# Performance work log

Measured on AMD Instinct MI355X. Metric: run time of the kernel, lower is better.

## Reference

```python
import jax, jax.numpy as jnp
import numpy as np

D, DFF, H, B, L, S = 1024, 4096, 16, 4, 1024, 1024


def setup_inputs() -> dict:
    key = jax.random.key(0)
    ks = jax.random.split(key, 8)
    w = lambda k, shape, s=0.02: jax.random.normal(k, shape, jnp.float32) * s
    return {
        'x': jax.random.normal(ks[0], (B, L, D), jnp.float32),
        'xa': jax.random.normal(ks[1], (B, S, D), jnp.float32),
        'sa_in_w': w(ks[2], (3 * D, D)), 'sa_in_b': jnp.zeros((3 * D,), jnp.float32),
        'sa_out_w': w(ks[3], (D, D)), 'sa_out_b': jnp.zeros((D,), jnp.float32),
        'ln1_w': jnp.ones((D,), jnp.float32), 'ln1_b': jnp.zeros((D,), jnp.float32),
        'ca_in_w': w(ks[4], (3 * D, D)), 'ca_in_b': jnp.zeros((3 * D,), jnp.float32),
        'ca_out_w': w(ks[5], (D, D)), 'ca_out_b': jnp.zeros((D,), jnp.float32),
        'ln2_w': jnp.ones((D,), jnp.float32), 'ln2_b': jnp.zeros((D,), jnp.float32),
        'ff_w1': w(ks[6], (DFF, D)), 'ff_b1': jnp.zeros((DFF,), jnp.float32),
        'ff_w2': w(ks[7], (D, DFF)), 'ff_b2': jnp.zeros((D,), jnp.float32),
        'ln3_w': jnp.ones((D,), jnp.float32), 'ln3_b': jnp.zeros((D,), jnp.float32),
    }


def layer_norm(x, w, b, eps=1e-5):
    m = x.mean(-1, keepdims=True)
    v = ((x - m) ** 2).mean(-1, keepdims=True)
    return (x - m) * jax.lax.rsqrt(v + eps) * w + b


def mha(q_in, kv_in, in_w, in_b, out_w, out_b):
    # torch MultiheadAttention eager path; returns (out, head-averaged weights)
    wq, wk, wv = jnp.split(in_w, 3, axis=0)
    bq, bk, bv = jnp.split(in_b, 3, axis=0)
    Bq, Lq, Dm = q_in.shape
    Lk = kv_in.shape[1]
    dh = Dm // H
    q = (q_in @ wq.T + bq).reshape(Bq, Lq, H, dh)
    k = (kv_in @ wk.T + bk).reshape(Bq, Lk, H, dh)
    v = (kv_in @ wv.T + bv).reshape(Bq, Lk, H, dh)
    scores = jnp.einsum('blhd,bshd->bhls', q, k) / jnp.sqrt(jnp.asarray(dh, q.dtype))
    attn = jax.nn.softmax(scores, axis=-1)  # [B,H,L,S]
    out = jnp.einsum('bhls,bshd->blhd', attn, v).reshape(Bq, Lq, Dm)
    return out @ out_w.T + out_b, attn.mean(axis=1)


def reference(x, xa, sa_in_w, sa_in_b, sa_out_w, sa_out_b, ln1_w, ln1_b,
              ca_in_w, ca_in_b, ca_out_w, ca_out_b, ln2_w, ln2_b,
              ff_w1, ff_b1, ff_w2, ff_b2, ln3_w, ln3_b):
    # NOTE: module overwrites x with LN(x) before the residual add
    x = layer_norm(x, ln1_w, ln1_b)
    a, self_w = mha(x, x, sa_in_w, sa_in_b, sa_out_w, sa_out_b)
    x = x + a
    x = layer_norm(x, ln2_w, ln2_b)
    a, cross_w = mha(x, xa, ca_in_w, ca_in_b, ca_out_w, ca_out_b)
    x = x + a
    h = layer_norm(x, ln3_w, ln3_b)
    x = x + (jax.nn.gelu(h @ ff_w1.T + ff_b1, approximate=False) @ ff_w2.T + ff_b2)
    return (x, jax.lax.stop_gradient(self_w), jax.lax.stop_gradient(cross_w))
```

## Files before the change

### kernel.cpp

```cpp
#include <hip/hip_runtime.h>
#include <cstdint>
#include <cstddef>


#define DEVI __device__ __forceinline__

typedef unsigned short u16;
typedef unsigned int u32;
typedef float f32x4 __attribute__((ext_vector_type(4)));
typedef short bf16x8 __attribute__((ext_vector_type(8)));

DEVI float bf2f(u16 u) { union { u32 i; float f; } x; x.i = ((u32)u) << 16; return x.f; }
DEVI u16 f2bf(float f) {
  union { float f; u32 i; } x; x.f = f;
  u32 r = x.i + 0x7fffu + ((x.i >> 16) & 1u);
  return (u16)(r >> 16);
}
DEVI u32 cvtpk(float lo, float hi) {
  u32 r;
  asm("v_cvt_pk_bf16_f32 %0, %1, %2" : "=v"(r) : "v"(lo), "v"(hi));
  return r;
}
DEVI float unplo(u32 u) { union { u32 i; float f; } x; x.i = u << 16; return x.f; }
DEVI float unphi(u32 u) { union { u32 i; float f; } x; x.i = u & 0xffff0000u; return x.f; }

typedef const __attribute__((address_space(1))) void GV;
typedef __attribute__((address_space(3))) void LV;
DEVI void glds16(const void* g, void* l) {
  __builtin_amdgcn_global_load_lds((GV*)g, (LV*)l, 16, 0, 0);
}

struct ConvBatch {
  const float* src[7];
  u16* dst[7];
  int n[7];
};

__global__ __launch_bounds__(256) void conv_batch(ConvBatch cb) {
  int t = blockIdx.y;
  const float* __restrict__ in = cb.src[t];
  u16* __restrict__ out = cb.dst[t];
  int n = cb.n[t];
  int i = (blockIdx.x * 256 + threadIdx.x) * 4;
  int stride = gridDim.x * 256 * 4;
  for (; i < n; i += stride) {
    float4 v = *(const float4*)(in + i);
    ushort4 o; o.x = f2bf(v.x); o.y = f2bf(v.y); o.z = f2bf(v.z); o.w = f2bf(v.w);
    *(ushort4*)(out + i) = o;
  }
}

__global__ __launch_bounds__(256) void ln_kernel(const float* __restrict__ in,
                                                 const float* __restrict__ gw,
                                                 const float* __restrict__ gb,
                                                 float* __restrict__ o32,
                                                 u16* __restrict__ o16) {
  int row = blockIdx.x;
  int t = threadIdx.x;
  const float* p = in + ((size_t)row << 10);
  float4 v = *(const float4*)(p + t * 4);
  float s = v.x + v.y + v.z + v.w;
  float q = v.x * v.x + v.y * v.y + v.z * v.z + v.w * v.w;
#pragma unroll
  for (int off = 32; off; off >>= 1) { s += __shfl_xor(s, off, 64); q += __shfl_xor(q, off, 64); }
  __shared__ float sb[8];
  int lane = t & 63, wv = t >> 6;
  if (!lane) { sb[wv] = s; sb[4 + wv] = q; }
  __syncthreads();
  s = sb[0] + sb[1] + sb[2] + sb[3];
  q = sb[4] + sb[5] + sb[6] + sb[7];
  float mean = s * (1.f / 1024.f);
  float var = q * (1.f / 1024.f) - mean * mean;
  float rs = rsqrtf(var + 1e-5f);
  float4 w4 = *(const float4*)(gw + t * 4);
  float4 b4 = *(const float4*)(gb + t * 4);
  float y0 = (v.x - mean) * rs * w4.x + b4.x;
  float y1 = (v.y - mean) * rs * w4.y + b4.y;
  float y2 = (v.z - mean) * rs * w4.z + b4.z;
  float y3 = (v.w - mean) * rs * w4.w + b4.w;
  float4 o; o.x = y0; o.y = y1; o.z = y2; o.w = y3;
  *(float4*)(o32 + ((size_t)row << 10) + t * 4) = o;
  ushort4 ob; ob.x = f2bf(y0); ob.y = f2bf(y1); ob.z = f2bf(y2); ob.w = f2bf(y3);
  *(ushort4*)(o16 + ((size_t)row << 10) + t * 4) = ob;
}

__global__ __launch_bounds__(256) void transpose_v(const u16* __restrict__ src, u16* __restrict__ dst) {
  __shared__ u16 tile[64][72];
  int bh = blockIdx.y;
  int b = bh >> 4, h = bh & 15;
  int s0 = blockIdx.x * 64;
  int t = threadIdx.x;
#pragma unroll
  for (int p = 0; p < 4; ++p) {
    int s = p * 16 + (t >> 4);
    int d = (t & 15) * 4;
    ushort4 v = *(const ushort4*)(src + ((size_t)(b * 1024 + s0 + s)) * 3072 + h * 64 + d);
    tile[s][d] = v.x; tile[s][d + 1] = v.y; tile[s][d + 2] = v.z; tile[s][d + 3] = v.w;
  }
  __syncthreads();
#pragma unroll
  for (int p = 0; p < 4; ++p) {
    int d = p * 16 + (t >> 4);
    int s = (t & 15) * 4;
    ushort4 v;
    v.x = tile[s][d]; v.y = tile[s + 1][d]; v.z = tile[s + 2][d]; v.w = tile[s + 3][d];
    *(ushort4*)(dst + ((size_t)(bh * 64 + d)) * 1024 + s0 + s) = v;
  }
}

__global__ __launch_bounds__(256, 4) void attn_fused2(const u16* __restrict__ qkv,
                                                      const u16* __restrict__ vT,
                                                      u16* __restrict__ probs,
                                                      u16* __restrict__ attnv) {
  __shared__ __align__(16) char LdsRaw[17408];
  __shared__ float wredm[4][2][16];
  __shared__ float wreds[4][2][16];
  u16* Kst = (u16*)LdsRaw;
  float* Ored = (float*)LdsRaw;

  const int hbid = blockIdx.y * 32 + blockIdx.x;
  const int lbid = (hbid & 7) * 256 + (hbid >> 3);
  const int z = lbid >> 5, b = z >> 4, h = z & 15;
  const int l0 = (lbid & 31) * 32;
  const int tid = threadIdx.x, lane = tid & 63, w = tid >> 6;
  const int fr = lane & 15, c16 = lane >> 4;

  bf16x8 qf[2][2];
#pragma unroll
  for (int i = 0; i < 2; ++i)
#pragma unroll
    for (int kk = 0; kk < 2; ++kk)
      qf[i][kk] = *(const bf16x8*)(qkv + (size_t)(b * 1024 + l0 + 16 * i + fr) * 3072 +
                                   h * 64 + kk * 32 + c16 * 8);

  const u16* Kbase = qkv + (size_t)b * 1024 * 3072 + 1024 + h * 64;

  u32 pk[2][16][2];
  float mx0 = -1e30f, mx1 = -1e30f;

#pragma unroll
  for (int cc = 0; cc < 8; ++cc) {
#pragma unroll
    for (int it = 0; it < 4; ++it) {
      int n = it * 256 + tid;
      int kk = n >> 9, r = (n >> 2) & 127, un = n & 3;
      int su = un ^ ((r >> 1) & 3);
      glds16(Kbase + (size_t)(cc * 128 + r) * 3072 + kk * 32 + su * 8, (char*)Kst + n * 16);
    }
    __syncthreads();

    f32x4 acc[2][2];
#pragma unroll
    for (int i = 0; i < 2; ++i)
#pragma unroll
      for (int sj = 0; sj < 2; ++sj) acc[i][sj] = (f32x4){0.f, 0.f, 0.f, 0.f};
#pragma unroll
    for (int kk = 0; kk < 2; ++kk) {
      bf16x8 kf[2];
#pragma unroll
      for (int sj = 0; sj < 2; ++sj) {
        int R = w * 32 + sj * 16 + fr;
        kf[sj] = *(const bf16x8*)((char*)Kst + kk * 8192 + R * 64 + ((c16 ^ ((R >> 1) & 3)) << 4));
      }
#pragma unroll
      for (int i = 0; i < 2; ++i)
#pragma unroll
        for (int sj = 0; sj < 2; ++sj)
          acc[i][sj] = __builtin_amdgcn_mfma_f32_16x16x32_bf16(kf[sj], qf[i][kk], acc[i][sj], 0, 0, 0);
    }
    __syncthreads();

#pragma unroll
    for (int sj = 0; sj < 2; ++sj) {
      f32x4 a0 = acc[0][sj], a1 = acc[1][sj];
      float v00 = a0[0] * 0.125f, v01 = a0[1] * 0.125f, v02 = a0[2] * 0.125f, v03 = a0[3] * 0.125f;
      float v10 = a1[0] * 0.125f, v11 = a1[1] * 0.125f, v12 = a1[2] * 0.125f, v13 = a1[3] * 0.125f;
      mx0 = fmaxf(mx0, fmaxf(fmaxf(v00, v01), fmaxf(v02, v03)));
      mx1 = fmaxf(mx1, fmaxf(fmaxf(v10, v11), fmaxf(v12, v13)));
      pk[0][cc * 2 + sj][0] = cvtpk(v00, v01); pk[0][cc * 2 + sj][1] = cvtpk(v02, v03);
      pk[1][cc * 2 + sj][0] = cvtpk(v10, v11); pk[1][cc * 2 + sj][1] = cvtpk(v12, v13);
    }
  }

  mx0 = fmaxf(mx0, __shfl_xor(mx0, 16, 64)); mx0 = fmaxf(mx0, __shfl_xor(mx0, 32, 64));
  mx1 = fmaxf(mx1, __shfl_xor(mx1, 16, 64)); mx1 = fmaxf(mx1, __shfl_xor(mx1, 32, 64));
  if (lane < 16) { wredm[w][0][fr] = mx0; wredm[w][1][fr] = mx1; }
  __syncthreads();
  float m0 = fmaxf(fmaxf(wredm[0][0][fr], wredm[1][0][fr]), fmaxf(wredm[2][0][fr], wredm[3][0][fr]));
  float m1 = fmaxf(fmaxf(wredm[0][1][fr], wredm[1][1][fr]), fmaxf(wredm[2][1][fr], wredm[3][1][fr]));

  const float L2E = 1.4426950408889634f;
  float mL0 = m0 * L2E, mL1 = m1 * L2E;
  float sm0 = 0.f, sm1 = 0.f;
#pragma unroll
  for (int idx = 0; idx < 16; ++idx) {
    u32 a0 = pk[0][idx][0], a1 = pk[0][idx][1];
    float p0 = exp2f(fmaf(unplo(a0), L2E, -mL0));
    float p1 = exp2f(fmaf(unphi(a0), L2E, -mL0));
    float p2 = exp2f(fmaf(unplo(a1), L2E, -mL0));
    float p3 = exp2f(fmaf(unphi(a1), L2E, -mL0));
    sm0 += (p0 + p1) + (p2 + p3);
    pk[0][idx][0] = cvtpk(p0, p1); pk[0][idx][1] = cvtpk(p2, p3);
    u32 b0 = pk[1][idx][0], b1 = pk[1][idx][1];
    float q0 = exp2f(fmaf(unplo(b0), L2E, -mL1));
    float q1 = exp2f(fmaf(unphi(b0), L2E, -mL1));
    float q2 = exp2f(fmaf(unplo(b1), L2E, -mL1));
    float q3 = exp2f(fmaf(unphi(b1), L2E, -mL1));
    sm1 += (q0 + q1) + (q2 + q3);
    pk[1][idx][0] = cvtpk(q0, q1); pk[1][idx][1] = cvtpk(q2, q3);
  }
  sm0 += __shfl_xor(sm0, 16, 64); sm0 += __shfl_xor(sm0, 32, 64);
  sm1 += __shfl_xor(sm1, 16, 64); sm1 += __shfl_xor(sm1, 32, 64);
  if (lane < 16) { wreds[w][0][fr] = sm0; wreds[w][1][fr] = sm1; }
  __syncthreads();
  float inv0 = 1.f / (wreds[0][0][fr] + wreds[1][0][fr] + wreds[2][0][fr] + wreds[3][0][fr]);
  float inv1 = 1.f / (wreds[0][1][fr] + wreds[1][1][fr] + wreds[2][1][fr] + wreds[3][1][fr]);

#pragma unroll
  for (int i = 0; i < 2; ++i) {
    float inv = i ? inv1 : inv0;
    u16* pg = probs + ((size_t)z << 20) + ((size_t)(l0 + 16 * i + fr) << 10);
#pragma unroll
    for (int cc = 0; cc < 8; ++cc)
#pragma unroll
      for (int sj = 0; sj < 2; ++sj) {
        int idx = cc * 2 + sj;
        u32 a0 = pk[i][idx][0], a1 = pk[i][idx][1];
        u32 n0 = cvtpk(unplo(a0) * inv, unphi(a0) * inv);
        u32 n1 = cvtpk(unplo(a1) * inv, unphi(a1) * inv);
        pk[i][idx][0] = n0; pk[i][idx][1] = n1;
        uint2 st; st.x = n0; st.y = n1;
        *(uint2*)(pg + cc * 128 + w * 32 + sj * 16 + c16 * 4) = st;
      }
  }

  f32x4 pacc[2][4];
#pragma unroll
  for (int i = 0; i < 2; ++i)
#pragma unroll
    for (int dj = 0; dj < 4; ++dj) pacc[i][dj] = (f32x4){0.f, 0.f, 0.f, 0.f};

  const u16* Vb = vT + ((size_t)z << 16);
  const int laneA = fr + ((c16 & 1) << 5);
  const int laneB = laneA + 16;
  const bool selhi = (c16 & 2) != 0;

#pragma unroll
  for (int cc = 0; cc < 8; ++cc) {
    const int sb = cc * 128 + w * 32;
    const int pidx = cc * 2;
    bf16x8 vf[4];
#pragma unroll
    for (int dj = 0; dj < 4; ++dj)
      vf[dj] = *(const bf16x8*)(Vb + (size_t)(16 * dj + fr) * 1024 + sb + c16 * 8);
#pragma unroll
    for (int i = 0; i < 2; ++i) {
      u32 sA0 = __shfl(pk[i][pidx][0], laneA, 64), sA1 = __shfl(pk[i][pidx][1], laneA, 64);
      u32 sA2 = __shfl(pk[i][pidx + 1][0], laneA, 64), sA3 = __shfl(pk[i][pidx + 1][1], laneA, 64);
      u32 sB0 = __shfl(pk[i][pidx][0], laneB, 64), sB1 = __shfl(pk[i][pidx][1], laneB, 64);
      u32 sB2 = __shfl(pk[i][pidx + 1][0], laneB, 64), sB3 = __shfl(pk[i][pidx + 1][1], laneB, 64);
      union { u32 u[4]; bf16x8 v; } A;
      A.u[0] = selhi ? sA2 : sA0;
      A.u[1] = selhi ? sA3 : sA1;
      A.u[2] = selhi ? sB2 : sB0;
      A.u[3] = selhi ? sB3 : sB1;
#pragma unroll
      for (int dj = 0; dj < 4; ++dj)
        pacc[i][dj] = __builtin_amdgcn_mfma_f32_16x16x32_bf16(A.v, vf[dj], pacc[i][dj], 0, 0, 0);
    }
  }

  if (w < 2) {
    float* Ow = Ored + w * (32 * 68);
#pragma unroll
    for (int i = 0; i < 2; ++i)
#pragma unroll
      for (int dj = 0; dj < 4; ++dj)
#pragma unroll
        for (int q = 0; q < 4; ++q)
          Ow[(16 * i + 4 * c16 + q) * 68 + 16 * dj + fr] = pacc[i][dj][q];
  }
  __syncthreads();
  if (w >= 2) {
    float* Ow = Ored + (w - 2) * (32 * 68);
#pragma unroll
    for (int i = 0; i < 2; ++i)
#pragma unroll
      for (int dj = 0; dj < 4; ++dj)
#pragma unroll
        for (int q = 0; q < 4; ++q)
          Ow[(16 * i + 4 * c16 + q) * 68 + 16 * dj + fr] += pacc[i][dj][q];
  }
  __syncthreads();

  {
    int l = tid >> 3, d0 = (tid & 7) * 8;
    float o[8];
#pragma unroll
    for (int e = 0; e < 8; ++e)
      o[e] = Ored[l * 68 + d0 + e] + Ored[32 * 68 + l * 68 + d0 + e];
    union { u32 u[4]; bf16x8 v; } O;
    O.u[0] = cvtpk(o[0], o[1]); O.u[1] = cvtpk(o[2], o[3]);
    O.u[2] = cvtpk(o[4], o[5]); O.u[3] = cvtpk(o[6], o[7]);
    *(bf16x8*)(attnv + ((size_t)b << 20) + (size_t)(l0 + l) * 1024 + h * 64 + d0) = O.v;
  }
}

__global__ __launch_bounds__(256) void mean_heads(const u16* __restrict__ probs, float* __restrict__ out) {
  int row = blockIdx.x;
  int b = row >> 10, l = row & 1023;
  int t = threadIdx.x;
  float4 a = {0.f, 0.f, 0.f, 0.f};
  const u16* base = probs + ((size_t)b << 24) + ((size_t)l << 10) + t * 4;
#pragma unroll
  for (int h = 0; h < 16; ++h) {
    ushort4 u = *(const ushort4*)(base + ((size_t)h << 20));
    a.x += bf2f(u.x); a.y += bf2f(u.y); a.z += bf2f(u.z); a.w += bf2f(u.w);
  }
  a.x *= 0.0625f; a.y *= 0.0625f; a.z *= 0.0625f; a.w *= 0.0625f;
  *(float4*)(out + ((size_t)row << 10) + t * 4) = a;
}

template <int BM, int BN, int WGM, int WGN, int EPI, bool O32, bool O16>
DEVI void gemm_core(const u16* __restrict__ A, int lda,
                    const u16* __restrict__ B, int ldb, int K,
                    const float* __restrict__ bias,
                    const float* __restrict__ resid,
                    float* __restrict__ C32, u16* __restrict__ C16, int ldc,
                    float scale, int m0, int n0) {
  constexpr int BK = 32;
  constexpr int WTM = BM / WGM;
  constexpr int WTN = BN / WGN;
  constexpr int FM = WTM / 16;
  constexpr int FN = WTN / 16;
  static_assert(BM % 64 == 0 && BN % 64 == 0, "staging granularity");

  __shared__ __align__(1024) u16 As[BM * BK];
  __shared__ __align__(1024) u16 Bs[BN * BK];

  const int tid = threadIdx.x;
  const int lane = tid & 63;
  const int wave = tid >> 6;
  const int wr = wave / WGN;
  const int wc = wave % WGN;

  f32x4 acc[FM][FN];
#pragma unroll
  for (int i = 0; i < FM; ++i)
#pragma unroll
    for (int j = 0; j < FN; ++j) acc[i][j] = (f32x4){0.f, 0.f, 0.f, 0.f};

  const int srow = tid >> 2;
  const int sunit = tid & 3;
  const int fr = lane & 15;
  const int c16 = lane >> 4;

  for (int kt = 0; kt < K; kt += BK) {
#pragma unroll
    for (int ch = 0; ch < BM / 64; ++ch) {
      int r = ch * 64 + srow;
      int gu = sunit ^ ((r >> 1) & 3);
      glds16(A + (size_t)(m0 + r) * lda + kt + gu * 8, (char*)As + ch * 4096 + tid * 16);
    }
#pragma unroll
    for (int ch = 0; ch < BN / 64; ++ch) {
      int r = ch * 64 + srow;
      int gu = sunit ^ ((r >> 1) & 3);
      glds16(B + (size_t)(n0 + r) * ldb + kt + gu * 8, (char*)Bs + ch * 4096 + tid * 16);
    }
    __syncthreads();

    bf16x8 af[FM], bfv[FN];
#pragma unroll
    for (int i = 0; i < FM; ++i) {
      int R = wr * WTM + i * 16 + fr;
      af[i] = *(const bf16x8*)((const char*)As + R * 64 + ((c16 ^ ((R >> 1) & 3)) << 4));
    }
#pragma unroll
    for (int j = 0; j < FN; ++j) {
      int R = wc * WTN + j * 16 + fr;
      bfv[j] = *(const bf16x8*)((const char*)Bs + R * 64 + ((c16 ^ ((R >> 1) & 3)) << 4));
    }
#pragma unroll
    for (int i = 0; i < FM; ++i)
#pragma unroll
      for (int j = 0; j < FN; ++j)
        acc[i][j] = __builtin_amdgcn_mfma_f32_16x16x32_bf16(af[i], bfv[j], acc[i][j], 0, 0, 0);
    __syncthreads();
  }

  const int orow = m0 + wr * WTM + (lane >> 4) * 4;
  const int ocol = n0 + wc * WTN + (lane & 15);
#pragma unroll
  for (int i = 0; i < FM; ++i) {
#pragma unroll
    for (int j = 0; j < FN; ++j) {
      int col = ocol + j * 16;
      float bv = bias ? bias[col] : 0.f;
#pragma unroll
      for (int q = 0; q < 4; ++q) {
        int row = orow + i * 16 + q;
        float v = acc[i][j][q] * scale + bv;
        if (EPI == 2) v = 0.5f * v * (1.0f + erff(v * 0.70710678118654752f));
        if (EPI == 1) v += resid[(size_t)row * ldc + col];
        if (O32) C32[(size_t)row * ldc + col] = v;
        if (O16) C16[(size_t)row * ldc + col] = f2bf(v);
      }
    }
  }
}

template <int BM, int BN, int WGM, int WGN, int EPI, bool O32, bool O16>
__global__ __launch_bounds__(256) void gemm_tn(const u16* __restrict__ A, int lda,
                                               const u16* __restrict__ B, int ldb, int K,
                                               const float* __restrict__ bias,
                                               const float* __restrict__ resid,
                                               float* __restrict__ C32, u16* __restrict__ C16,
                                               int ldc, float scale) {
  gemm_core<BM, BN, WGM, WGN, EPI, O32, O16>(A, lda, B, ldb, K, bias, resid, C32, C16, ldc, scale,
                                             blockIdx.y * BM, blockIdx.x * BN);
}

__global__ __launch_bounds__(256) void gemm_splitk_ff2(const u16* __restrict__ A,
                                                       const u16* __restrict__ B,
                                                       float* __restrict__ part) {
  int z = blockIdx.z;
  gemm_core<128, 128, 2, 2, 0, true, false>(A + z * 1024, 4096, B + z * 1024, 4096, 1024, nullptr,
                                            nullptr, part + (size_t)z * 4194304, nullptr, 1024, 1.f,
                                            blockIdx.y * 128, blockIdx.x * 128);
}

__global__ __launch_bounds__(256) void reduce_ff2(const float* __restrict__ part,
                                                  const float* __restrict__ bias,
                                                  const float* __restrict__ resid,
                                                  float* __restrict__ out) {
  size_t i = ((size_t)blockIdx.x * 256 + threadIdx.x) * 4;
  float4 s0 = *(const float4*)(part + i);
  float4 s1 = *(const float4*)(part + 4194304 + i);
  float4 s2 = *(const float4*)(part + 8388608 + i);
  float4 s3 = *(const float4*)(part + 12582912 + i);
  int col = (int)(i & 1023);
  float4 bv = *(const float4*)(bias + col);
  float4 rv = *(const float4*)(resid + i);
  float4 o;
  o.x = s0.x + s1.x + s2.x + s3.x + bv.x + rv.x;
  o.y = s0.y + s1.y + s2.y + s3.y + bv.y + rv.y;
  o.z = s0.z + s1.z + s2.z + s3.z + bv.z + rv.z;
  o.w = s0.w + s1.w + s2.w + s3.w + bv.w + rv.w;
  *(float4*)(out + i) = o;
}

extern "C" void kernel_launch(void* const* d_in, const int* in_sizes, int n_in,
                              void* d_out, int out_size, void* d_ws, size_t ws_size,
                              hipStream_t stream) {
  const float* x       = (const float*)d_in[0];
  const float* xa      = (const float*)d_in[1];
  const float* sa_in_w = (const float*)d_in[2];
  const float* sa_in_b = (const float*)d_in[3];
  const float* sa_out_w= (const float*)d_in[4];
  const float* sa_out_b= (const float*)d_in[5];
  const float* ln1_w   = (const float*)d_in[6];
  const float* ln1_b   = (const float*)d_in[7];
  const float* ca_in_w = (const float*)d_in[8];
  const float* ca_in_b = (const float*)d_in[9];
  const float* ca_out_w= (const float*)d_in[10];
  const float* ca_out_b= (const float*)d_in[11];
  const float* ln2_w   = (const float*)d_in[12];
  const float* ln2_b   = (const float*)d_in[13];
  const float* ff_w1   = (const float*)d_in[14];
  const float* ff_b1   = (const float*)d_in[15];
  const float* ff_w2   = (const float*)d_in[16];
  const float* ff_b2   = (const float*)d_in[17];
  const float* ln3_w   = (const float*)d_in[18];
  const float* ln3_b   = (const float*)d_in[19];

  float* out_x     = (float*)d_out;
  float* out_self  = out_x + 4194304;
  float* out_cross = out_x + 8388608;

  char* w = (char*)d_ws;
  u16*   wb_sa_in  = (u16*)(w + 0);
  u16*   wb_sa_out = (u16*)(w + 6291456);
  u16*   wb_ca_in  = (u16*)(w + 8388608);
  u16*   wb_ca_out = (u16*)(w + 14680064);
  u16*   wb_ff1    = (u16*)(w + 16777216);
  u16*   wb_ff2    = (u16*)(w + 25165824);
  float* t32       = (float*)(w + 33554432);
  u16*   t16       = (u16*)(w + 50331648);
  float* x_acc     = (float*)(w + 58720256);
  u16*   qkv       = (u16*)(w + 75497472);
  u16*   vT        = (u16*)(w + 100663296);
  u16*   attnv     = (u16*)(w + 109051904);
  u16*   xa16      = (u16*)(w + 117440512);
  u16*   probs     = (u16*)(w + 125829120);
  u16*   ff1       = probs;
  float* part      = (float*)(w + 159383552);

  dim3 blk(256);

  ConvBatch cb;
  cb.src[0] = sa_in_w;  cb.dst[0] = wb_sa_in;  cb.n[0] = 3145728;
  cb.src[1] = sa_out_w; cb.dst[1] = wb_sa_out; cb.n[1] = 1048576;
  cb.src[2] = ca_in_w;  cb.dst[2] = wb_ca_in;  cb.n[2] = 3145728;
  cb.src[3] = ca_out_w; cb.dst[3] = wb_ca_out; cb.n[3] = 1048576;
  cb.src[4] = ff_w1;    cb.dst[4] = wb_ff1;    cb.n[4] = 4194304;
  cb.src[5] = ff_w2;    cb.dst[5] = wb_ff2;    cb.n[5] = 4194304;
  cb.src[6] = xa;       cb.dst[6] = xa16;      cb.n[6] = 4194304;
  conv_batch<<<dim3(512, 7), blk, 0, stream>>>(cb);

  ln_kernel<<<dim3(4096), blk, 0, stream>>>(x, ln1_w, ln1_b, t32, t16);
  gemm_tn<128, 128, 2, 2, 0, false, true><<<dim3(24, 32), blk, 0, stream>>>(
      t16, 1024, wb_sa_in, 1024, 1024, sa_in_b, nullptr, nullptr, qkv, 3072, 1.f);
  transpose_v<<<dim3(16, 64), blk, 0, stream>>>(qkv + 2048, vT);
  attn_fused2<<<dim3(32, 64), blk, 0, stream>>>(qkv, vT, probs, attnv);
  mean_heads<<<dim3(4096), blk, 0, stream>>>(probs, out_self);
  gemm_tn<64, 128, 2, 2, 1, true, false><<<dim3(8, 64), blk, 0, stream>>>(
      attnv, 1024, wb_sa_out, 1024, 1024, sa_out_b, t32, x_acc, nullptr, 1024, 1.f);

  ln_kernel<<<dim3(4096), blk, 0, stream>>>(x_acc, ln2_w, ln2_b, t32, t16);
  gemm_tn<64, 128, 2, 2, 0, false, true><<<dim3(8, 64), blk, 0, stream>>>(
      t16, 1024, wb_ca_in, 1024, 1024, ca_in_b, nullptr, nullptr, qkv, 3072, 1.f);
  gemm_tn<128, 128, 2, 2, 0, false, true><<<dim3(16, 32), blk, 0, stream>>>(
      xa16, 1024, wb_ca_in + 1048576, 1024, 1024, ca_in_b + 1024, nullptr, nullptr, qkv + 1024, 3072, 1.f);
  transpose_v<<<dim3(16, 64), blk, 0, stream>>>(qkv + 2048, vT);
  attn_fused2<<<dim3(32, 64), blk, 0, stream>>>(qkv, vT, probs, attnv);
  mean_heads<<<dim3(4096), blk, 0, stream>>>(probs, out_cross);
  gemm_tn<64, 128, 2, 2, 1, true, false><<<dim3(8, 64), blk, 0, stream>>>(
      attnv, 1024, wb_ca_out, 1024, 1024, ca_out_b, t32, x_acc, nullptr, 1024, 1.f);

  ln_kernel<<<dim3(4096), blk, 0, stream>>>(x_acc, ln3_w, ln3_b, t32, t16);
  gemm_tn<128, 128, 2, 2, 2, false, true><<<dim3(32, 32), blk, 0, stream>>>(
      t16, 1024, wb_ff1, 1024, 1024, ff_b1, nullptr, nullptr, ff1, 4096, 1.f);
  gemm_splitk_ff2<<<dim3(8, 32, 4), blk, 0, stream>>>(ff1, wb_ff2, part);
  reduce_ff2<<<dim3(4096), blk, 0, stream>>>(part, ff_b2, x_acc, out_x);
}
```

Before: 589.5 us.

## Double-buffer K tiles in attention and widen mean_heads loads

Result: no change. 584.7 us (-0.8%).

```diff
diff --git a/kernel.cpp b/kernel.cpp
--- a/kernel.cpp
+++ b/kernel.cpp
@@ -112,10 +112,9 @@
                                                       const u16* __restrict__ vT,
                                                       u16* __restrict__ probs,
                                                       u16* __restrict__ attnv) {
-  __shared__ __align__(16) char LdsRaw[17408];
+  __shared__ __align__(16) char LdsRaw[32768];
   __shared__ float wredm[4][2][16];
   __shared__ float wreds[4][2][16];
-  u16* Kst = (u16*)LdsRaw;
   float* Ored = (float*)LdsRaw;
 
   const int hbid = blockIdx.y * 32 + blockIdx.x;
@@ -139,15 +138,27 @@
   float mx0 = -1e30f, mx1 = -1e30f;
 
 #pragma unroll
+  for (int it = 0; it < 4; ++it) {
+    int n = it * 256 + tid;
+    int kk = n >> 9, r = (n >> 2) & 127, un = n & 3;
+    int su = un ^ ((r >> 1) & 3);
+    glds16(Kbase + (size_t)r * 3072 + kk * 32 + su * 8, LdsRaw + n * 16);
+  }
+  __syncthreads();
+
+#pragma unroll
   for (int cc = 0; cc < 8; ++cc) {
-#pragma unroll
-    for (int it = 0; it < 4; ++it) {
-      int n = it * 256 + tid;
-      int kk = n >> 9, r = (n >> 2) & 127, un = n & 3;
-      int su = un ^ ((r >> 1) & 3);
-      glds16(Kbase + (size_t)(cc * 128 + r) * 3072 + kk * 32 + su * 8, (char*)Kst + n * 16);
-    }
-    __syncthreads();
+    char* cur = LdsRaw + (cc & 1) * 16384;
+    if (cc < 7) {
+      char* nxt = LdsRaw + ((cc + 1) & 1) * 16384;
+#pragma unroll
+      for (int it = 0; it < 4; ++it) {
+        int n = it * 256 + tid;
+        int kk = n >> 9, r = (n >> 2) & 127, un = n & 3;
+        int su = un ^ ((r >> 1) & 3);
+        glds16(Kbase + (size_t)((cc + 1) * 128 + r) * 3072 + kk * 32 + su * 8, nxt + n * 16);
+      }
+    }
 
     f32x4 acc[2][2];
 #pragma unroll
@@ -160,7 +171,7 @@
 #pragma unroll
       for (int sj = 0; sj < 2; ++sj) {
         int R = w * 32 + sj * 16 + fr;
-        kf[sj] = *(const bf16x8*)((char*)Kst + kk * 8192 + R * 64 + ((c16 ^ ((R >> 1) & 3)) << 4));
+        kf[sj] = *(const bf16x8*)(cur + kk * 8192 + R * 64 + ((c16 ^ ((R >> 1) & 3)) << 4));
       }
 #pragma unroll
       for (int i = 0; i < 2; ++i)
@@ -168,7 +179,6 @@
         for (int sj = 0; sj < 2; ++sj)
           acc[i][sj] = __builtin_amdgcn_mfma_f32_16x16x32_bf16(kf[sj], qf[i][kk], acc[i][sj], 0, 0, 0);
     }
-    __syncthreads();
 
 #pragma unroll
     for (int sj = 0; sj < 2; ++sj) {
@@ -180,6 +190,7 @@
       pk[0][cc * 2 + sj][0] = cvtpk(v00, v01); pk[0][cc * 2 + sj][1] = cvtpk(v02, v03);
       pk[1][cc * 2 + sj][0] = cvtpk(v10, v11); pk[1][cc * 2 + sj][1] = cvtpk(v12, v13);
     }
+    __syncthreads();
   }
 
   mx0 = fmaxf(mx0, __shfl_xor(mx0, 16, 64)); mx0 = fmaxf(mx0, __shfl_xor(mx0, 32, 64));
@@ -270,6 +281,7 @@
     }
   }
 
+  __syncthreads();
   if (w < 2) {
     float* Ow = Ored + w * (32 * 68);
 #pragma unroll
@@ -307,18 +319,25 @@
 }
 
 __global__ __launch_bounds__(256) void mean_heads(const u16* __restrict__ probs, float* __restrict__ out) {
-  int row = blockIdx.x;
-  int b = row >> 10, l = row & 1023;
-  int t = threadIdx.x;
-  float4 a = {0.f, 0.f, 0.f, 0.f};
-  const u16* base = probs + ((size_t)b << 24) + ((size_t)l << 10) + t * 4;
+  int r = blockIdx.x * 2 + (threadIdx.x >> 7);
+  int b = r >> 10, l = r & 1023;
+  int t = threadIdx.x & 127;
+  float a[8];
+#pragma unroll
+  for (int e = 0; e < 8; ++e) a[e] = 0.f;
+  const u16* base = probs + ((size_t)b << 24) + ((size_t)l << 10) + t * 8;
 #pragma unroll
   for (int h = 0; h < 16; ++h) {
-    ushort4 u = *(const ushort4*)(base + ((size_t)h << 20));
-    a.x += bf2f(u.x); a.y += bf2f(u.y); a.z += bf2f(u.z); a.w += bf2f(u.w);
-  }
-  a.x *= 0.0625f; a.y *= 0.0625f; a.z *= 0.0625f; a.w *= 0.0625f;
-  *(float4*)(out + ((size_t)row << 10) + t * 4) = a;
+    bf16x8 v = *(const bf16x8*)(base + ((size_t)h << 20));
+#pragma unroll
+    for (int e = 0; e < 8; ++e) a[e] += bf2f((u16)v[e]);
+  }
+  float4 o0, o1;
+  o0.x = a[0] * 0.0625f; o0.y = a[1] * 0.0625f; o0.z = a[2] * 0.0625f; o0.w = a[3] * 0.0625f;
+  o1.x = a[4] * 0.0625f; o1.y = a[5] * 0.0625f; o1.z = a[6] * 0.0625f; o1.w = a[7] * 0.0625f;
+  float* op = out + ((size_t)r << 10) + t * 8;
+  *(float4*)op = o0;
+  *(float4*)(op + 4) = o1;
 }
 
 template <int BM, int BN, int WGM, int WGN, int EPI, bool O32, bool O16>
@@ -513,7 +532,7 @@
       t16, 1024, wb_sa_in, 1024, 1024, sa_in_b, nullptr, nullptr, qkv, 3072, 1.f);
   transpose_v<<<dim3(16, 64), blk, 0, stream>>>(qkv + 2048, vT);
   attn_fused2<<<dim3(32, 64), blk, 0, stream>>>(qkv, vT, probs, attnv);
-  mean_heads<<<dim3(4096), blk, 0, stream>>>(probs, out_self);
+  mean_heads<<<dim3(2048), blk, 0, stream>>>(probs, out_self);
   gemm_tn<64, 128, 2, 2, 1, true, false><<<dim3(8, 64), blk, 0, stream>>>(
       attnv, 1024, wb_sa_out, 1024, 1024, sa_out_b, t32, x_acc, nullptr, 1024, 1.f);
 
@@ -524,7 +543,7 @@
       xa16, 1024, wb_ca_in + 1048576, 1024, 1024, ca_in_b + 1024, nullptr, nullptr, qkv + 1024, 3072, 1.f);
   transpose_v<<<dim3(16, 64), blk, 0, stream>>>(qkv + 2048, vT);
   attn_fused2<<<dim3(32, 64), blk, 0, stream>>>(qkv, vT, probs, attnv);
-  mean_heads<<<dim3(4096), blk, 0, stream>>>(probs, out_cross);
+  mean_heads<<<dim3(2048), blk, 0, stream>>>(probs, out_cross);
   gemm_tn<64, 128, 2, 2, 1, true, false><<<dim3(8, 64), blk, 0, stream>>>(
       attnv, 1024, wb_ca_out, 1024, 1024, ca_out_b, t32, x_acc, nullptr, 1024, 1.f);
 
```
